# Optimization experiments

Hardware: AMD Instinct MI355X
Metric: run time of the kernel (lower is better)

## Reference

```python
import jax, jax.numpy as jnp
import numpy as np

H = W = 256          # input_img_height (square images)
N_NODES = 8          # camera graph nodes
N_EDGES = 64         # ~fully connected directed graph
FEAT = 1024          # edge_feat_dim
BN_EPS = 1e-5


def setup_inputs() -> dict:
    key = jax.random.key(0)
    ks = jax.random.split(key, 8)
    d = {}
    d["x"] = jax.random.normal(ks[0], (N_NODES, 3 * H * W), dtype=jnp.float32)
    d["edge_index"] = jax.random.randint(ks[1], (2, N_EDGES), 0, N_NODES)
    # ResNet stem params (conv1 replaced to take 6 channels)
    d["conv1_w"] = jax.random.normal(ks[2], (64, 6, 7, 7), dtype=jnp.float32) * 0.05
    d["bn_gamma"] = jnp.ones((64,), jnp.float32)
    d["bn_beta"] = jnp.zeros((64,), jnp.float32)
    d["bn_mean"] = jnp.zeros((64,), jnp.float32)
    d["bn_var"] = jnp.ones((64,), jnp.float32)
    d["fc_w"] = jax.random.normal(ks[3], (FEAT, 64), dtype=jnp.float32) * 0.05
    d["fc_b"] = jnp.zeros((FEAT,), jnp.float32)
    d["fc_xyz_w"] = jax.random.normal(ks[4], (3, FEAT), dtype=jnp.float32) * 0.05
    d["fc_xyz_b"] = jnp.zeros((3,), jnp.float32)
    d["fc_wpqr_w"] = jax.random.normal(ks[5], (3, FEAT), dtype=jnp.float32) * 0.05
    d["fc_wpqr_b"] = jnp.zeros((3,), jnp.float32)
    return d


def _edge_extractor(ef, conv1_w, bn_gamma, bn_beta, bn_mean, bn_var, fc_w, fc_b):
    # conv1: 6->64, 7x7, stride 2, pad 3, no bias
    y = jax.lax.conv_general_dilated(
        ef, conv1_w, window_strides=(2, 2), padding=[(3, 3), (3, 3)],
        dimension_numbers=("NCHW", "OIHW", "NCHW"))
    # BatchNorm (inference form with running stats), fused scale/shift
    scale = (bn_gamma * jax.lax.rsqrt(bn_var + BN_EPS))[None, :, None, None]
    shift = (bn_beta - bn_mean * bn_gamma * jax.lax.rsqrt(bn_var + BN_EPS))[None, :, None, None]
    y = jax.nn.relu(y * scale + shift)
    # maxpool 3x3 stride 2 pad 1
    y = jax.lax.reduce_window(y, -jnp.inf, jax.lax.max,
                              (1, 1, 3, 3), (1, 1, 2, 2),
                              [(0, 0), (0, 0), (1, 1), (1, 1)])
    # AdaptiveAvgPool2d(1) + fc to edge_feat_dim
    y = jnp.mean(y, axis=(2, 3))                     # [E, 64]
    return y @ fc_w.T + fc_b                         # [E, FEAT]


def reference(x, edge_index, conv1_w, bn_gamma, bn_beta, bn_mean, bn_var,
              fc_w, fc_b, fc_xyz_w, fc_xyz_b, fc_wpqr_w, fc_wpqr_b):
    imgs = x.reshape(N_NODES, 3, H, W)
    # compute_edge_features, vectorized: gather min/max node per edge, concat channels
    nmin = jnp.min(edge_index, axis=0)               # [E]
    nmax = jnp.max(edge_index, axis=0)               # [E]
    edge_feat = jnp.concatenate([imgs[nmin], imgs[nmax]], axis=1)  # [E, 6, H, W]
    ef = _edge_extractor(edge_feat, conv1_w, bn_gamma, bn_beta, bn_mean, bn_var, fc_w, fc_b)
    ef = jax.nn.relu(ef)
    # droprate == 0 -> no dropout
    xyz = ef @ fc_xyz_w.T + fc_xyz_b                 # [E, 3]
    wpqr = ef @ fc_wpqr_w.T + fc_wpqr_b              # [E, 3]
    full = jnp.concatenate([xyz, wpqr], axis=1)      # [E, 6]
    return (full[:N_NODES], full)
```

## Files before the change

### kernel.cpp

```cpp
#include <hip/hip_runtime.h>
#include <hip/hip_bf16.h>

#define N_NODES 8
#define N_EDGES 64
#define CO 64
#define OH 128
#define OW 128
#define FEAT 1024
#define BN_EPS 1e-5f

#define OFF_PARTIAL 0
#define OFF_XPAD    151552
#define OFF_WB      3471616
#define OFF_A       3520768
#define OFF_B       20297984

#define RS_W 136
#define XROW 132

typedef short bf16x8 __attribute__((ext_vector_type(8)));
typedef float f32x4  __attribute__((ext_vector_type(4)));

__device__ __forceinline__ unsigned short f2bf(float f) {
    unsigned u = __float_as_uint(f);
    u += 0x7fffu + ((u >> 16) & 1u);
    return (unsigned short)(u >> 16);
}
__device__ __forceinline__ float blo(unsigned u) { return __uint_as_float(u << 16); }
__device__ __forceinline__ float bhi(unsigned u) { return __uint_as_float(u & 0xffff0000u); }

__global__ __launch_bounds__(256) void prep_kernel(
        const float* __restrict__ x, const float* __restrict__ w,
        const float* __restrict__ gamma, const float* __restrict__ var,
        unsigned* __restrict__ xpad, unsigned short* __restrict__ wb2) {
    int idx = blockIdx.x * 256 + threadIdx.x;
    if (idx < 8 * 3 * 262 * XROW) {
        int u   = idx % XROW;
        int r   = idx / XROW;
        int iyp = r % 262;
        int nc  = r / 262;
        int iy  = iyp - 3;
        unsigned val = 0u;
        if ((unsigned)iy < 256u) {
            int c0 = 2 * u - 3;
            const float* row = x + (size_t)nc * 65536 + iy * 256;
            float f0 = ((unsigned)c0 < 256u) ? row[c0] : 0.f;
            float f1 = ((unsigned)(c0 + 1) < 256u) ? row[c0 + 1] : 0.f;
            val = (unsigned)f2bf(f0) | ((unsigned)f2bf(f1) << 16);
        }
        xpad[idx] = val;
    }
    if (idx < 2 * 64 * 192) {
        int tp = idx % 192;
        int c  = (idx / 192) & 63;
        int h  = idx / (192 * 64);
        int rr = tp >> 3, kx = tp & 7;
        float val = 0.f;
        if (rr < 21 && kx < 7) {
            int ci = rr / 7, ky = rr % 7;
            float sc = gamma[c] * rsqrtf(var[c] + BN_EPS);
            val = w[((c * 6 + h * 3 + ci) * 7 + ky) * 7 + kx] * sc;
        }
        wb2[(rr * 128 + h * 64 + c) * 8 + kx] = f2bf(val);
    }
}

__global__ __launch_bounds__(1024, 4) void conv_kernel(
        const unsigned* __restrict__ xpad, const unsigned short* __restrict__ wb2,
        const float* __restrict__ gamma, const float* __restrict__ beta,
        const float* __restrict__ mean,  const float* __restrict__ var,
        unsigned short* __restrict__ A2, unsigned short* __restrict__ B2) {
    int bx  = blockIdx.x;
    int r16 = bx & 7;
    int idx = bx >> 3;
    int n   = idx >> 4;
    int oy  = (r16 << 4) + (idx & 15);
    int t   = threadIdx.x;

    __shared__ __align__(16) char smem[32768];
    unsigned* rawu = (unsigned*)smem;

    const unsigned* src = xpad + (size_t)n * (3 * 262 * XROW);
    if (t < 816) {
        int g  = t % 34;
        int rr = t / 34;
        uint4 v = make_uint4(0u, 0u, 0u, 0u);
        if (rr < 21 && g < 33) {
            int ci = (rr * 147) >> 10;
            int ky = rr - ci * 7;
            v = *(const uint4*)(src + (ci * 262 + 2 * oy + ky) * XROW + 4 * g);
        }
        *(uint4*)&rawu[rr * RS_W + 4 * g] = v;
    }
    __syncthreads();

    int wv = t >> 6, lane = t & 63;
    int h   = wv & 1;
    int wg  = (wv >> 1) & 3;
    int cth = wv >> 3;
    int quad = lane >> 4, m = lane & 15;

    f32x4 acc[2][2];
#pragma unroll
    for (int ctl = 0; ctl < 2; ++ctl) {
        acc[ctl][0] = (f32x4){0.f, 0.f, 0.f, 0.f};
        acc[ctl][1] = (f32x4){0.f, 0.f, 0.f, 0.f};
    }

    const bf16x8* wbv = (const bf16x8*)wb2;

#pragma unroll 2
    for (int s = 0; s < 6; ++s) {
        int rq = 4 * s + quad;
        bf16x8 afrag[2];
#pragma unroll
        for (int nt = 0; nt < 2; ++nt) {
            int ox = 32 * wg + 16 * nt + m;
            int base = rq * RS_W + ox;
            union { unsigned u[4]; bf16x8 v; } bb;
            bb.u[0] = rawu[base];     bb.u[1] = rawu[base + 1];
            bb.u[2] = rawu[base + 2]; bb.u[3] = rawu[base + 3];
            afrag[nt] = bb.v;
        }
#pragma unroll
        for (int ctl = 0; ctl < 2; ++ctl) {
            int ct = 2 * cth + ctl;
            bf16x8 wfrag = wbv[rq * 128 + h * 64 + 16 * ct + m];
#pragma unroll
            for (int nt = 0; nt < 2; ++nt)
                acc[ctl][nt] = __builtin_amdgcn_mfma_f32_16x16x32_bf16(
                                   afrag[nt], wfrag, acc[ctl][nt], 0, 0, 0);
        }
    }

    float sh[2] = {0.f, 0.f};
    if (h) {
#pragma unroll
        for (int ctl = 0; ctl < 2; ++ctl) {
            int c = 16 * (2 * cth + ctl) + m;
            float sc = gamma[c] * rsqrtf(var[c] + BN_EPS);
            sh[ctl] = beta[c] - mean[c] * sc;
        }
    }

    __syncthreads();
    unsigned short* T = (unsigned short*)smem;

#pragma unroll
    for (int ctl = 0; ctl < 2; ++ctl) {
        int chp = h * 64 + 16 * (2 * cth + ctl) + m;
        int sw  = (chp & 7) << 2;
#pragma unroll
        for (int nt = 0; nt < 2; ++nt) {
            int px0 = 32 * wg + 16 * nt + 4 * quad;
            float v0 = acc[ctl][nt][0] + sh[ctl];
            float v1 = acc[ctl][nt][1] + sh[ctl];
            float v2 = acc[ctl][nt][2] + sh[ctl];
            float v3 = acc[ctl][nt][3] + sh[ctl];
            uint2 pk;
            pk.x = (unsigned)f2bf(v0) | ((unsigned)f2bf(v1) << 16);
            pk.y = (unsigned)f2bf(v2) | ((unsigned)f2bf(v3) << 16);
            int gs = ((px0 >> 2) ^ sw);
            *(uint2*)&T[chp * 128 + gs * 4] = pk;
        }
    }
    __syncthreads();

    int row = t >> 3, slot = t & 7;
    int hh = row >> 6, ch = row & 63;
    int swr = (row & 7) << 2;
    unsigned short* dst = (hh ? B2 : A2)
                        + ((size_t)(n * CO + ch) << 14) + (oy << 7) + slot * 16;
#pragma unroll
    for (int i = 0; i < 2; ++i) {
        int g  = slot * 4 + i * 2;
        int gs = g ^ swr;
        *(uint4*)(dst + i * 8) = *(uint4*)&T[row * 128 + gs * 4];
    }
}

__global__ __launch_bounds__(256, 4) void pool_kernel(
        const unsigned short* __restrict__ A2,
        const unsigned short* __restrict__ B2,
        float* __restrict__ partial) {
    int pb  = blockIdx.x;
    int xcd = pb & 7;
    int q   = pb >> 3;
    int c   = q >> 1;
    int rt  = xcd * 2 + (q & 1);
    int t   = threadIdx.x;

    __shared__ unsigned short S[2 * 8 * 9 * 128];

    for (int k = t; k < 2304; k += 256) {
        int slot = k & 15;
        int r    = (k >> 4) % 9;
        int tn   = (k >> 4) / 9;
        int grow = 8 * rt - 1 + r;
        uint4 v = make_uint4(0u, 0u, 0u, 0u);
        if (grow >= 0) {
            const unsigned short* src = (tn >= 8) ? B2 : A2;
            int node = tn & 7;
            v = *(const uint4*)(src + ((size_t)(node * CO + c) << 14)
                                    + (grow << 7) + slot * 8);
        }
        *(uint4*)&S[tn * 1152 + (r << 7) + slot * 8] = v;
    }
    __syncthreads();

    int wv = t >> 6, lane = t & 63;
    int esub = lane >> 4, tc = lane & 15;

    for (int i = 0; i < 3; ++i) {
        int sidx = 12 * wv + 4 * i + esub;
        bool valid = sidx < 36;
        int ss = valid ? sidx : 0;
        int pi = 0, rem = ss;
        while (rem >= 8 - pi) { rem -= 8 - pi; ++pi; }
        int pj = pi + rem;
        const unsigned short* pa  = &S[pi * 1152];
        const unsigned short* pb2 = &S[(8 + pj) * 1152];

        float mx[4][4];
#pragma unroll
        for (int p = 0; p < 4; ++p)
#pragma unroll
            for (int qq = 0; qq < 4; ++qq) mx[p][qq] = 0.f;

#pragma unroll
        for (int r = 0; r < 9; ++r) {
            uint4 ga = *(const uint4*)(pa + (r << 7) + tc * 8);
            uint4 gb = *(const uint4*)(pb2 + (r << 7) + tc * 8);
            float ha = 0.f, hb = 0.f;
            if (tc > 0) {
                ha = bhi(*(const unsigned*)(pa + (r << 7) + tc * 8 - 2));
                hb = bhi(*(const unsigned*)(pb2 + (r << 7) + tc * 8 - 2));
            }
            float z0 = ha + hb;
            float z1 = blo(ga.x) + blo(gb.x), z2 = bhi(ga.x) + bhi(gb.x);
            float z3 = blo(ga.y) + blo(gb.y), z4 = bhi(ga.y) + bhi(gb.y);
            float z5 = blo(ga.z) + blo(gb.z), z6 = bhi(ga.z) + bhi(gb.z);
            float z7 = blo(ga.w) + blo(gb.w), z8 = bhi(ga.w) + bhi(gb.w);
            float h0 = fmaxf(fmaxf(z0, z1), z2);
            float h1 = fmaxf(fmaxf(z2, z3), z4);
            float h2 = fmaxf(fmaxf(z4, z5), z6);
            float h3 = fmaxf(fmaxf(z6, z7), z8);
            if (r & 1) {
                int p = (r - 1) >> 1;
                mx[p][0] = fmaxf(mx[p][0], h0); mx[p][1] = fmaxf(mx[p][1], h1);
                mx[p][2] = fmaxf(mx[p][2], h2); mx[p][3] = fmaxf(mx[p][3], h3);
            } else {
                if (r >= 2) {
                    int p = (r >> 1) - 1;
                    mx[p][0] = fmaxf(mx[p][0], h0); mx[p][1] = fmaxf(mx[p][1], h1);
                    mx[p][2] = fmaxf(mx[p][2], h2); mx[p][3] = fmaxf(mx[p][3], h3);
                }
                if (r <= 6) {
                    int p = r >> 1;
                    mx[p][0] = fmaxf(mx[p][0], h0); mx[p][1] = fmaxf(mx[p][1], h1);
                    mx[p][2] = fmaxf(mx[p][2], h2); mx[p][3] = fmaxf(mx[p][3], h3);
                }
            }
        }

        float sum = 0.f;
#pragma unroll
        for (int p = 0; p < 4; ++p)
#pragma unroll
            for (int qq = 0; qq < 4; ++qq) sum += fmaxf(mx[p][qq], 0.f);

        sum += __shfl_down(sum, 8, 64);
        sum += __shfl_down(sum, 4, 64);
        sum += __shfl_down(sum, 2, 64);
        sum += __shfl_down(sum, 1, 64);
        if (tc == 0 && valid)
            partial[(rt * 36 + sidx) * 64 + c] = sum;
    }
}

__global__ __launch_bounds__(256) void head_kernel(
        const int* __restrict__ ei, const float* __restrict__ partial,
        const float* __restrict__ fc_w,   const float* __restrict__ fc_b,
        const float* __restrict__ xyz_w,  const float* __restrict__ xyz_b,
        const float* __restrict__ wpqr_w, const float* __restrict__ wpqr_b,
        float* __restrict__ out) {
    int e = blockIdx.x;
    int t = threadIdx.x;
    int a0 = ei[e], a1 = ei[N_EDGES + e];
    int pi = min(a0, a1), pj = max(a0, a1);
    int rank = pi * 8 - ((pi * (pi + 1)) >> 1) + pj;
    __shared__ float pl[CO];
    if (t < CO) {
        float s = 0.f;
#pragma unroll
        for (int rt = 0; rt < 16; ++rt)
            s += partial[(rt * 36 + rank) * 64 + t];
        pl[t] = s * (1.f / 4096.f);
    }
    __syncthreads();

    float s[6] = {0.f, 0.f, 0.f, 0.f, 0.f, 0.f};
#pragma unroll
    for (int ff = 0; ff < 4; ++ff) {
        int f = ff * 256 + t;
        const float* wr = fc_w + f * CO;
        float d = fc_b[f];
#pragma unroll
        for (int c = 0; c < CO; ++c) d = fmaf(pl[c], wr[c], d);
        d = fmaxf(d, 0.f);
#pragma unroll
        for (int r = 0; r < 3; ++r) {
            s[r]     = fmaf(d, xyz_w[r * FEAT + f],  s[r]);
            s[3 + r] = fmaf(d, wpqr_w[r * FEAT + f], s[3 + r]);
        }
    }
#pragma unroll
    for (int r = 0; r < 6; ++r)
#pragma unroll
        for (int off = 32; off > 0; off >>= 1)
            s[r] += __shfl_down(s[r], off, 64);

    __shared__ float red[4][6];
    if ((t & 63) == 0) {
#pragma unroll
        for (int r = 0; r < 6; ++r) red[t >> 6][r] = s[r];
    }
    __syncthreads();
    if (t < 6) {
        float v = red[0][t] + red[1][t] + red[2][t] + red[3][t];
        v += (t < 3) ? xyz_b[t] : wpqr_b[t - 3];
        out[48 + e * 6 + t] = v;
        if (e < 8) out[e * 6 + t] = v;
    }
}

extern "C" void kernel_launch(void* const* d_in, const int* in_sizes, int n_in,
                              void* d_out, int out_size, void* d_ws, size_t ws_size,
                              hipStream_t stream) {
    const float* x        = (const float*)d_in[0];
    const int*   ei       = (const int*)d_in[1];
    const float* conv1_w  = (const float*)d_in[2];
    const float* bn_gamma = (const float*)d_in[3];
    const float* bn_beta  = (const float*)d_in[4];
    const float* bn_mean  = (const float*)d_in[5];
    const float* bn_var   = (const float*)d_in[6];
    const float* fc_w     = (const float*)d_in[7];
    const float* fc_b     = (const float*)d_in[8];
    const float* xyz_w    = (const float*)d_in[9];
    const float* xyz_b    = (const float*)d_in[10];
    const float* wpqr_w   = (const float*)d_in[11];
    const float* wpqr_b   = (const float*)d_in[12];
    float* out = (float*)d_out;

    char* ws = (char*)d_ws;
    float*          partial = (float*)(ws + OFF_PARTIAL);
    unsigned*       xpad    = (unsigned*)(ws + OFF_XPAD);
    unsigned short* wb2     = (unsigned short*)(ws + OFF_WB);
    unsigned short* A2      = (unsigned short*)(ws + OFF_A);
    unsigned short* B2      = (unsigned short*)(ws + OFF_B);

    int img_work = 8 * 3 * 262 * XROW;
    prep_kernel<<<(img_work + 255) / 256, 256, 0, stream>>>(
        x, conv1_w, bn_gamma, bn_var, xpad, wb2);
    conv_kernel<<<1024, 1024, 0, stream>>>(xpad, wb2, bn_gamma, bn_beta,
                                           bn_mean, bn_var, A2, B2);
    pool_kernel<<<1024, 256, 0, stream>>>(A2, B2, partial);
    head_kernel<<<64, 256, 0, stream>>>(ei, partial, fc_w, fc_b,
                                        xyz_w, xyz_b, wpqr_w, wpqr_b, out);
}
```

Before: 129.5 us.

## Enlarge per-wave conv tiles with 256-thread blocks and transpose fc weights for head

The conv kernel drops from 1024 to 256 threads per block. Each wave now computes a 4x4 grid of MFMA tiles instead of 2x2, so it reuses its A and weight fragments across more tiles and issues fewer LDS and global loads per MFMA. The head kernel now runs 1024 threads, one output feature per thread. It reads an fc weight copy that the prep kernel transposes, which makes the loads coalesced. In exchange, each thread holds more accumulator registers, fewer waves are resident to hide latency, and prep does an extra transpose pass.

```diff
diff --git a/kernel.cpp b/kernel.cpp
--- a/kernel.cpp
+++ b/kernel.cpp
@@ -14,6 +14,7 @@
 #define OFF_WB      3471616
 #define OFF_A       3520768
 #define OFF_B       20297984
+#define OFF_FCWT    37075200
 
 #define RS_W 136
 #define XROW 132
@@ -32,7 +33,9 @@
 __global__ __launch_bounds__(256) void prep_kernel(
         const float* __restrict__ x, const float* __restrict__ w,
         const float* __restrict__ gamma, const float* __restrict__ var,
-        unsigned* __restrict__ xpad, unsigned short* __restrict__ wb2) {
+        const float* __restrict__ fc_w,
+        unsigned* __restrict__ xpad, unsigned short* __restrict__ wb2,
+        float* __restrict__ fc_wT) {
     int idx = blockIdx.x * 256 + threadIdx.x;
     if (idx < 8 * 3 * 262 * XROW) {
         int u   = idx % XROW;
@@ -63,9 +66,13 @@
         }
         wb2[(rr * 128 + h * 64 + c) * 8 + kx] = f2bf(val);
     }
-}
-
-__global__ __launch_bounds__(1024, 4) void conv_kernel(
+    if (idx < CO * FEAT) {
+        int c = idx >> 10, f = idx & 1023;
+        fc_wT[idx] = fc_w[f * CO + c];
+    }
+}
+
+__global__ __launch_bounds__(256, 3) void conv_kernel(
         const unsigned* __restrict__ xpad, const unsigned short* __restrict__ wb2,
         const float* __restrict__ gamma, const float* __restrict__ beta,
         const float* __restrict__ mean,  const float* __restrict__ var,
@@ -81,9 +88,9 @@
     unsigned* rawu = (unsigned*)smem;
 
     const unsigned* src = xpad + (size_t)n * (3 * 262 * XROW);
-    if (t < 816) {
-        int g  = t % 34;
-        int rr = t / 34;
+    for (int k = t; k < 816; k += 256) {
+        int g  = k % 34;
+        int rr = k / 34;
         uint4 v = make_uint4(0u, 0u, 0u, 0u);
         if (rr < 21 && g < 33) {
             int ci = (rr * 147) >> 10;
@@ -95,27 +102,26 @@
     __syncthreads();
 
     int wv = t >> 6, lane = t & 63;
-    int h   = wv & 1;
-    int wg  = (wv >> 1) & 3;
-    int cth = wv >> 3;
+    int hg = wv >> 1;
+    int wg = wv & 1;
     int quad = lane >> 4, m = lane & 15;
 
-    f32x4 acc[2][2];
-#pragma unroll
-    for (int ctl = 0; ctl < 2; ++ctl) {
-        acc[ctl][0] = (f32x4){0.f, 0.f, 0.f, 0.f};
-        acc[ctl][1] = (f32x4){0.f, 0.f, 0.f, 0.f};
-    }
+    f32x4 acc[4][4];
+#pragma unroll
+    for (int ct = 0; ct < 4; ++ct)
+#pragma unroll
+        for (int nt = 0; nt < 4; ++nt)
+            acc[ct][nt] = (f32x4){0.f, 0.f, 0.f, 0.f};
 
     const bf16x8* wbv = (const bf16x8*)wb2;
 
 #pragma unroll 2
     for (int s = 0; s < 6; ++s) {
         int rq = 4 * s + quad;
-        bf16x8 afrag[2];
-#pragma unroll
-        for (int nt = 0; nt < 2; ++nt) {
-            int ox = 32 * wg + 16 * nt + m;
+        bf16x8 afrag[4];
+#pragma unroll
+        for (int nt = 0; nt < 4; ++nt) {
+            int ox = 64 * wg + 16 * nt + m;
             int base = rq * RS_W + ox;
             union { unsigned u[4]; bf16x8 v; } bb;
             bb.u[0] = rawu[base];     bb.u[1] = rawu[base + 1];
@@ -123,23 +129,22 @@
             afrag[nt] = bb.v;
         }
 #pragma unroll
-        for (int ctl = 0; ctl < 2; ++ctl) {
-            int ct = 2 * cth + ctl;
-            bf16x8 wfrag = wbv[rq * 128 + h * 64 + 16 * ct + m];
-#pragma unroll
-            for (int nt = 0; nt < 2; ++nt)
-                acc[ctl][nt] = __builtin_amdgcn_mfma_f32_16x16x32_bf16(
-                                   afrag[nt], wfrag, acc[ctl][nt], 0, 0, 0);
-        }
-    }
-
-    float sh[2] = {0.f, 0.f};
-    if (h) {
-#pragma unroll
-        for (int ctl = 0; ctl < 2; ++ctl) {
-            int c = 16 * (2 * cth + ctl) + m;
+        for (int ct = 0; ct < 4; ++ct) {
+            bf16x8 wfrag = wbv[rq * 128 + hg * 64 + 16 * ct + m];
+#pragma unroll
+            for (int nt = 0; nt < 4; ++nt)
+                acc[ct][nt] = __builtin_amdgcn_mfma_f32_16x16x32_bf16(
+                                  afrag[nt], wfrag, acc[ct][nt], 0, 0, 0);
+        }
+    }
+
+    float sh[4] = {0.f, 0.f, 0.f, 0.f};
+    if (hg) {
+#pragma unroll
+        for (int ct = 0; ct < 4; ++ct) {
+            int c = 16 * ct + m;
             float sc = gamma[c] * rsqrtf(var[c] + BN_EPS);
-            sh[ctl] = beta[c] - mean[c] * sc;
+            sh[ct] = beta[c] - mean[c] * sc;
         }
     }
 
@@ -147,16 +152,16 @@
     unsigned short* T = (unsigned short*)smem;
 
 #pragma unroll
-    for (int ctl = 0; ctl < 2; ++ctl) {
-        int chp = h * 64 + 16 * (2 * cth + ctl) + m;
+    for (int ct = 0; ct < 4; ++ct) {
+        int chp = hg * 64 + 16 * ct + m;
         int sw  = (chp & 7) << 2;
 #pragma unroll
-        for (int nt = 0; nt < 2; ++nt) {
-            int px0 = 32 * wg + 16 * nt + 4 * quad;
-            float v0 = acc[ctl][nt][0] + sh[ctl];
-            float v1 = acc[ctl][nt][1] + sh[ctl];
-            float v2 = acc[ctl][nt][2] + sh[ctl];
-            float v3 = acc[ctl][nt][3] + sh[ctl];
+        for (int nt = 0; nt < 4; ++nt) {
+            int px0 = 64 * wg + 16 * nt + 4 * quad;
+            float v0 = acc[ct][nt][0] + sh[ct];
+            float v1 = acc[ct][nt][1] + sh[ct];
+            float v2 = acc[ct][nt][2] + sh[ct];
+            float v3 = acc[ct][nt][3] + sh[ct];
             uint2 pk;
             pk.x = (unsigned)f2bf(v0) | ((unsigned)f2bf(v1) << 16);
             pk.y = (unsigned)f2bf(v2) | ((unsigned)f2bf(v3) << 16);
@@ -166,16 +171,19 @@
     }
     __syncthreads();
 
-    int row = t >> 3, slot = t & 7;
-    int hh = row >> 6, ch = row & 63;
-    int swr = (row & 7) << 2;
-    unsigned short* dst = (hh ? B2 : A2)
-                        + ((size_t)(n * CO + ch) << 14) + (oy << 7) + slot * 16;
-#pragma unroll
-    for (int i = 0; i < 2; ++i) {
-        int g  = slot * 4 + i * 2;
-        int gs = g ^ swr;
-        *(uint4*)(dst + i * 8) = *(uint4*)&T[row * 128 + gs * 4];
+#pragma unroll
+    for (int rr = 0; rr < 4; ++rr) {
+        int row = rr * 32 + (t >> 3), slot = t & 7;
+        int hh = row >> 6, ch = row & 63;
+        int swr = (row & 7) << 2;
+        unsigned short* dst = (hh ? B2 : A2)
+                            + ((size_t)(n * CO + ch) << 14) + (oy << 7) + slot * 16;
+#pragma unroll
+        for (int i = 0; i < 2; ++i) {
+            int g  = slot * 4 + i * 2;
+            int gs = g ^ swr;
+            *(uint4*)(dst + i * 8) = *(uint4*)&T[row * 128 + gs * 4];
+        }
     }
 }
 
@@ -278,9 +286,9 @@
     }
 }
 
-__global__ __launch_bounds__(256) void head_kernel(
+__global__ __launch_bounds__(1024) void head_kernel(
         const int* __restrict__ ei, const float* __restrict__ partial,
-        const float* __restrict__ fc_w,   const float* __restrict__ fc_b,
+        const float* __restrict__ fc_wT,  const float* __restrict__ fc_b,
         const float* __restrict__ xyz_w,  const float* __restrict__ xyz_b,
         const float* __restrict__ wpqr_w, const float* __restrict__ wpqr_b,
         float* __restrict__ out) {
@@ -299,20 +307,17 @@
     }
     __syncthreads();
 
-    float s[6] = {0.f, 0.f, 0.f, 0.f, 0.f, 0.f};
-#pragma unroll
-    for (int ff = 0; ff < 4; ++ff) {
-        int f = ff * 256 + t;
-        const float* wr = fc_w + f * CO;
-        float d = fc_b[f];
-#pragma unroll
-        for (int c = 0; c < CO; ++c) d = fmaf(pl[c], wr[c], d);
-        d = fmaxf(d, 0.f);
-#pragma unroll
-        for (int r = 0; r < 3; ++r) {
-            s[r]     = fmaf(d, xyz_w[r * FEAT + f],  s[r]);
-            s[3 + r] = fmaf(d, wpqr_w[r * FEAT + f], s[3 + r]);
-        }
+    float d = fc_b[t];
+#pragma unroll
+    for (int c = 0; c < CO; ++c)
+        d = fmaf(pl[c], fc_wT[c * FEAT + t], d);
+    d = fmaxf(d, 0.f);
+
+    float s[6];
+#pragma unroll
+    for (int r = 0; r < 3; ++r) {
+        s[r]     = d * xyz_w[r * FEAT + t];
+        s[3 + r] = d * wpqr_w[r * FEAT + t];
     }
 #pragma unroll
     for (int r = 0; r < 6; ++r)
@@ -320,14 +325,16 @@
         for (int off = 32; off > 0; off >>= 1)
             s[r] += __shfl_down(s[r], off, 64);
 
-    __shared__ float red[4][6];
+    __shared__ float red[16][6];
     if ((t & 63) == 0) {
 #pragma unroll
         for (int r = 0; r < 6; ++r) red[t >> 6][r] = s[r];
     }
     __syncthreads();
     if (t < 6) {
-        float v = red[0][t] + red[1][t] + red[2][t] + red[3][t];
+        float v = 0.f;
+#pragma unroll
+        for (int w = 0; w < 16; ++w) v += red[w][t];
         v += (t < 3) ? xyz_b[t] : wpqr_b[t - 3];
         out[48 + e * 6 + t] = v;
         if (e < 8) out[e * 6 + t] = v;
@@ -358,13 +365,14 @@
     unsigned short* wb2     = (unsigned short*)(ws + OFF_WB);
     unsigned short* A2      = (unsigned short*)(ws + OFF_A);
     unsigned short* B2      = (unsigned short*)(ws + OFF_B);
+    float*          fc_wT   = (float*)(ws + OFF_FCWT);
 
     int img_work = 8 * 3 * 262 * XROW;
     prep_kernel<<<(img_work + 255) / 256, 256, 0, stream>>>(
-        x, conv1_w, bn_gamma, bn_var, xpad, wb2);
-    conv_kernel<<<1024, 1024, 0, stream>>>(xpad, wb2, bn_gamma, bn_beta,
-                                           bn_mean, bn_var, A2, B2);
+        x, conv1_w, bn_gamma, bn_var, fc_w, xpad, wb2, fc_wT);
+    conv_kernel<<<1024, 256, 0, stream>>>(xpad, wb2, bn_gamma, bn_beta,
+                                          bn_mean, bn_var, A2, B2);
     pool_kernel<<<1024, 256, 0, stream>>>(A2, B2, partial);
-    head_kernel<<<64, 256, 0, stream>>>(ei, partial, fc_w, fc_b,
-                                        xyz_w, xyz_b, wpqr_w, wpqr_b, out);
-}
+    head_kernel<<<64, 1024, 0, stream>>>(ei, partial, fc_wT, fc_b,
+                                         xyz_w, xyz_b, wpqr_w, wpqr_b, out);
+}
```

After: 119.4 us. 1.09x faster.
